# Performance work log

Hardware: AMD Instinct MI355X
Metric: run time of the kernel (lower is better)

Reference implementation:

```python
import jax, jax.numpy as jnp
from jax import lax
import numpy as np

WIN = 7            # skimage structural_similarity default win_size
K1, K2 = 0.01, 0.03
DATA_RANGE = 1.0


def _mean_filter_valid(x, win):
    k = jnp.ones((1, 1, win, win), x.dtype) / (win * win)
    y = lax.conv_general_dilated(x[:, None], k, (1, 1), 'VALID')
    return y[:, 0]


def ssim_loss(img1, img2):
    # img1, img2: (B, H, W); skimage-style SSIM, mean over batch of (1 - ssim)
    f = lambda z: _mean_filter_valid(z, WIN)
    NP = WIN * WIN
    cov_norm = NP / (NP - 1.0)  # unbiased estimator, as in skimage
    ux, uy = f(img1), f(img2)
    uxx, uyy, uxy = f(img1 * img1), f(img2 * img2), f(img1 * img2)
    vx = cov_norm * (uxx - ux * ux)
    vy = cov_norm * (uyy - uy * uy)
    vxy = cov_norm * (uxy - ux * uy)
    C1 = (K1 * DATA_RANGE) ** 2
    C2 = (K2 * DATA_RANGE) ** 2
    S = ((2 * ux * uy + C1) * (2 * vxy + C2)) / ((ux * ux + uy * uy + C1) * (vx + vy + C2))
    return jnp.mean(1.0 - jnp.mean(S, axis=(1, 2)))


def conv2d_same(x, w, b):
    # x: (B, Cin, H, W), w: (Cout, Cin, 3, 3)
    y = lax.conv_general_dilated(x, w, (1, 1), 'SAME')
    return y + b[None, :, None, None]


def maxpool2(x):
    return lax.reduce_window(x, -jnp.inf, lax.max, (1, 1, 2, 2), (1, 1, 2, 2), 'VALID')


def features(x, w1, b1, w2, b2, w3, b3, w4, b4):
    h = jax.nn.relu(conv2d_same(x, w1, b1))
    h = jax.nn.relu(conv2d_same(h, w2, b2))
    h = maxpool2(h)
    h = jax.nn.relu(conv2d_same(h, w3, b3))
    h = jax.nn.relu(conv2d_same(h, w4, b4))
    return h


def _conv_init(key, cout, cin, k=3):
    # torch Conv2d default init: U(-s, s), s = 1/sqrt(cin*k*k)
    kw, kb = jax.random.split(key)
    s = 1.0 / np.sqrt(cin * k * k)
    w = jax.random.uniform(kw, (cout, cin, k, k), jnp.float32, -s, s)
    b = jax.random.uniform(kb, (cout,), jnp.float32, -s, s)
    return w, b


def setup_inputs() -> dict:
    key = jax.random.key(0)
    ks = jax.random.split(key, 6)
    B, H, W = 8, 256, 256
    sr = jax.random.uniform(ks[0], (B, 1, H, W), jnp.float32)
    hr = jax.random.uniform(ks[1], (B, 1, H, W), jnp.float32)
    w1, b1 = _conv_init(ks[2], 64, 1)
    w2, b2 = _conv_init(ks[3], 128, 64)
    w3, b3 = _conv_init(ks[4], 256, 128)
    w4, b4 = _conv_init(ks[5], 256, 256)
    return {"sr": sr, "hr": hr, "w1": w1, "b1": b1, "w2": w2, "b2": b2,
            "w3": w3, "b3": b3, "w4": w4, "b4": b4}


def reference(sr, hr, w1, b1, w2, b2, w3, b3, w4, b4):
    mse_weight, ssim_weight, perceptual_weight = 1.0, 0.5, 0.1
    mse = jnp.mean((sr - hr) ** 2)
    # torch detaches before SSIM (numpy round-trip) -> no gradient through SSIM
    ssim_l = ssim_loss(lax.stop_gradient(sr[:, 0]), lax.stop_gradient(hr[:, 0]))
    sr_f = features(sr, w1, b1, w2, b2, w3, b3, w4, b4)
    hr_f = features(hr, w1, b1, w2, b2, w3, b3, w4, b4)
    perceptual = jnp.mean((sr_f - hr_f) ** 2)
    total = mse_weight * mse + ssim_weight * ssim_l + perceptual_weight * perceptual
    return total, mse, ssim_l, perceptual
```

## Files before the change

### kernel.cpp

```cpp
#include <hip/hip_runtime.h>
#include <hip/hip_bf16.h>

typedef __hip_bfloat16 bf16;
typedef unsigned char u8;
typedef __attribute__((ext_vector_type(4))) float f32x4;
typedef __attribute__((ext_vector_type(8))) int i32x8;
typedef __attribute__((ext_vector_type(4))) unsigned int u32x4;

struct L4 { long a, b, c, d; };
struct U2 { u32x4 x, y; };

typedef __attribute__((address_space(3))) unsigned int lds_uint;
typedef __attribute__((address_space(1))) const unsigned int g_uint;
__device__ inline void gload_lds16(const void* g, void* l) {
    __builtin_amdgcn_global_load_lds((g_uint*)g, (lds_uint*)l, 16, 0, 0);
}

__device__ inline void block_reduce_atomic(float v, float* dst) {
    #pragma unroll
    for (int o = 32; o > 0; o >>= 1) v += __shfl_down(v, o, 64);
    __shared__ float ws[8];
    const int lane = threadIdx.x & 63;
    const int wid  = threadIdx.x >> 6;
    if (lane == 0) ws[wid] = v;
    __syncthreads();
    if (threadIdx.x == 0) {
        float s = 0.f;
        const int nw = (blockDim.x + 63) >> 6;
        for (int i = 0; i < nw; ++i) s += ws[i];
        atomicAdd(dst, s);
    }
}

__global__ void prep_loss_kernel(
    const float* __restrict__ w2, u8* __restrict__ wb2,
    const float* __restrict__ w3, u8* __restrict__ wb3,
    const float* __restrict__ w4, u8* __restrict__ wb4,
    const float* __restrict__ x, const float* __restrict__ y,
    float* __restrict__ accs) {
    const int blk = blockIdx.x;
    if (blk < 3744) {
        const float* w; u8* wb; int CIN, CO, idx;
        if (blk < 288)       { w = w2; wb = wb2; CIN = 64;  CO = 128; idx = blk * 256 + threadIdx.x; }
        else if (blk < 1440) { w = w3; wb = wb3; CIN = 128; CO = 256; idx = (blk - 288) * 256 + threadIdx.x; }
        else                 { w = w4; wb = wb4; CIN = 256; CO = 256; idx = (blk - 1440) * 256 + threadIdx.x; }
        int n = CO * 9 * CIN;
        if (idx >= n) return;
        int t = idx % 9;
        int rest = idx / 9;
        int ci = rest % CIN;
        int co = rest / CIN;
        float v = w[idx];
        int p = ci >> 5, c32 = ci & 31;
        size_t off = (size_t)p * 288 * CO;
        if (t < 8) off += (((size_t)t * 2 + (c32 >> 4)) * CO + co) * 16 + (c32 & 15);
        else       off += 256 * (size_t)CO + (((size_t)(c32 >> 4)) * CO + co) * 16 + (c32 & 15);
        int r = __builtin_amdgcn_cvt_pk_fp8_f32(v, v, 0, false);
        wb[off] = (u8)(r & 0xff);
        return;
    }
    const int lb = blk - 3744;
    float val = 0.f;
    float* dst;
    if (lb < 1960) {
        dst = accs + 1;
        const int b = lb / 245;
        const int t = (lb - b * 245) * 256 + threadIdx.x;
        if (t < 250 * 250) {
            const int i = t / 250, j = t - (t / 250) * 250;
            const float* xp = x + (size_t)b * 65536;
            const float* yp = y + (size_t)b * 65536;
            float sx = 0.f, sy = 0.f, sxx = 0.f, syy = 0.f, sxy = 0.f;
            #pragma unroll
            for (int dy = 0; dy < 7; ++dy) {
                const float* xr = xp + (size_t)(i + dy) * 256 + j;
                const float* yr = yp + (size_t)(i + dy) * 256 + j;
                #pragma unroll
                for (int dx = 0; dx < 7; ++dx) {
                    float a = xr[dx], c = yr[dx];
                    sx += a; sy += c;
                    sxx += a * a; syy += c * c; sxy += a * c;
                }
            }
            const float inv = 1.f / 49.f;
            const float cn  = 49.f / 48.f;
            float ux = sx * inv, uy = sy * inv;
            float vx  = cn * (sxx * inv - ux * ux);
            float vy  = cn * (syy * inv - uy * uy);
            float vxy = cn * (sxy * inv - ux * uy);
            const float C1 = 1e-4f, C2 = 9e-4f;
            val = ((2.f * ux * uy + C1) * (2.f * vxy + C2)) /
                  ((ux * ux + uy * uy + C1) * (vx + vy + C2));
        }
    } else {
        dst = accs + 0;
        int i = (lb - 1960) * 256 + threadIdx.x;
        float4 a = ((const float4*)x)[i];
        float4 b = ((const float4*)y)[i];
        float d0 = a.x - b.x, d1 = a.y - b.y, d2 = a.z - b.z, d3 = a.w - b.w;
        val = d0 * d0 + d1 * d1 + d2 * d2 + d3 * d3;
    }
    block_reduce_atomic(val, dst);
}

__global__ void finalize_kernel(const float* __restrict__ accs, float* __restrict__ out) {
    if (threadIdx.x == 0) {
        float mse    = accs[0] * (1.f / 524288.f);
        float ssim_l = 1.f - accs[1] * (1.f / 500000.f);
        float perc   = accs[2] * (1.f / 33554432.f);
        out[0] = mse + 0.5f * ssim_l + 0.1f * perc;
        out[1] = mse;
        out[2] = ssim_l;
        out[3] = perc;
    }
}

__global__ __launch_bounds__(256) void conv1_kernel(
    const float* __restrict__ sr, const float* __restrict__ hr, int nb, int b0,
    const float* __restrict__ w, const float* __restrict__ bias,
    u8* __restrict__ out) {
    const int H = 256, W = 256;
    const int img = blockIdx.y;
    const float* in = (img < nb) ? (sr + (size_t)(b0 + img) * 65536)
                                 : (hr + (size_t)(b0 + img - nb) * 65536);
    int px = blockIdx.x * 256 + threadIdx.x;
    int y = px >> 8, x = px & 255;
    float p[9];
    #pragma unroll
    for (int dy = 0; dy < 3; ++dy)
        #pragma unroll
        for (int dx = 0; dx < 3; ++dx) {
            int gy = y + dy - 1, gx = x + dx - 1;
            float v = 0.f;
            if ((unsigned)gy < (unsigned)H && (unsigned)gx < (unsigned)W)
                v = in[(size_t)gy * W + gx];
            p[dy * 3 + dx] = v;
        }
    #pragma unroll
    for (int g = 0; g < 8; ++g) {
        float v[8];
        #pragma unroll
        for (int c = 0; c < 8; ++c) {
            int co = g * 8 + c;
            float a = bias[co];
            #pragma unroll
            for (int k = 0; k < 9; ++k) a += w[co * 9 + k] * p[k];
            v[c] = fmaxf(a, 0.f);
        }
        uint2 o;
        int r;
        r = __builtin_amdgcn_cvt_pk_fp8_f32(v[0], v[1], 0, false);
        o.x = __builtin_amdgcn_cvt_pk_fp8_f32(v[2], v[3], r, true);
        r = __builtin_amdgcn_cvt_pk_fp8_f32(v[4], v[5], 0, false);
        o.y = __builtin_amdgcn_cvt_pk_fp8_f32(v[6], v[7], r, true);
        *(uint2*)(out + (((size_t)img * 8 + g) * 65536 + px) * 8) = o;
    }
}

#define BUF_SZ   32768
#define N_ACT_CH 720
#define N_CHUNK  1872
#define WT_BOFF  11520

__global__ __launch_bounds__(256, 2) void conv2_ss(
    const u8* __restrict__ in, const u8* __restrict__ wb,
    const float* __restrict__ bias, u8* __restrict__ out,
    const float* __restrict__ zbuf) {
    const int H = 256, W = 256, CO = 128;
    const size_t HW = 65536;
    const int tid  = threadIdx.x;
    const int lane = tid & 63;
    const int wn   = tid >> 6;
    const int xl = lane & 15;
    const int kq = lane >> 4;
    const int x0 = blockIdx.x * 16;
    const int y0 = blockIdx.y * 16;
    const int img = blockIdx.z >> 1;
    const int co0 = (blockIdx.z & 1) << 6;

    __shared__ __align__(16) char smem[59904];

    f32x4 acc[4][4];
    #pragma unroll
    for (int m = 0; m < 4; ++m)
        #pragma unroll
        for (int n = 0; n < 4; ++n) acc[m][n] = (f32x4){0.f, 0.f, 0.f, 0.f};

    const u8* inp = in + (size_t)img * 8 * HW * 8;

    {
        char* d = smem + tid * 16;
        #pragma unroll
        for (int i = 0; i < 15; ++i) {
            int c = tid + i * 256;
            if (c >= 2 * N_CHUNK) break;
            int ph = (c >= N_CHUNK) ? 1 : 0;
            int c2 = c - ph * N_CHUNK;
            const char* src = (const char*)zbuf;
            if (c2 < N_ACT_CH) {
                int g = c2 / 180, r = c2 - g * 180;
                int row = r / 10, pp = r - row * 10;
                int gy = y0 - 1 + row, colb = x0 - 2 + pp * 2;
                if ((unsigned)gy < (unsigned)H && (unsigned)colb < (unsigned)(W - 1))
                    src = (const char*)(inp + (((size_t)(g + ph * 4)) * HW +
                                              (size_t)gy * W + colb) * 8);
            } else {
                int c3 = c2 - N_ACT_CH;
                size_t o;
                if (c3 < 1024) {
                    int gt = c3 >> 6, co = c3 & 63;
                    o = ((size_t)gt * CO + co0 + co) * 16;
                } else {
                    int c4 = c3 - 1024;
                    int q = c4 >> 6, co = c4 & 63;
                    o = 256 * (size_t)CO + ((size_t)q * CO + co0 + co) * 16;
                }
                src = (const char*)(wb + (size_t)ph * 288 * CO + o);
            }
            gload_lds16(src, d + i * 4096);
        }
    }

    int mxo[2];
    #pragma unroll
    for (int g = 0; g < 2; ++g) {
        int t = g * 4 + kq;
        int dy = t / 3, dx = t - dy * 3;
        mxo[g] = (dy * 20 + dx) * 8;
    }
    const int abase = ((wn * 4) * 20 + xl + 1) * 8;
    const int awmx  = WT_BOFF + kq * 2048 + xl * 16;
    const int aw8   = WT_BOFF + 16384 + (kq >> 1) * 1024 + xl * 16 + (kq & 1) * 8;
    const int ab8   = kq * 2880 + abase + (2 * 20 + 2) * 8;

    __syncthreads();

    #pragma unroll
    for (int p = 0; p < 2; ++p) {
        const char* base = smem + p * 29952;
        #pragma unroll
        for (int g = 0; g < 2; ++g) {
            i32x8 A[4];
            #pragma unroll
            for (int mt = 0; mt < 4; ++mt) {
                const char* pa = base + awmx + g * 8192 + mt * 256;
                U2 u{*(const u32x4*)pa, *(const u32x4*)(pa + 1024)};
                A[mt] = __builtin_bit_cast(i32x8, u);
            }
            #pragma unroll
            for (int nt = 0; nt < 4; ++nt) {
                const char* pb = base + abase + mxo[g] + nt * 160;
                L4 l{*(const long*)pb, *(const long*)(pb + 2880),
                     *(const long*)(pb + 5760), *(const long*)(pb + 8640)};
                i32x8 B = __builtin_bit_cast(i32x8, l);
                #pragma unroll
                for (int mt = 0; mt < 4; ++mt)
                    acc[mt][nt] = __builtin_amdgcn_mfma_scale_f32_16x16x128_f8f6f4(
                        A[mt], B, acc[mt][nt], 0, 0,
                        0, 0x7F7F7F7F, 0, 0x7F7F7F7F);
            }
        }
        {
            long A8[4], B8[4];
            #pragma unroll
            for (int mt = 0; mt < 4; ++mt)
                A8[mt] = *(const long*)(base + aw8 + mt * 256);
            #pragma unroll
            for (int nt = 0; nt < 4; ++nt)
                B8[nt] = *(const long*)(base + ab8 + nt * 160);
            #pragma unroll
            for (int mt = 0; mt < 4; ++mt)
                #pragma unroll
                for (int nt = 0; nt < 4; ++nt)
                    acc[mt][nt] = __builtin_amdgcn_mfma_f32_16x16x32_fp8_fp8(
                        A8[mt], B8[nt], acc[mt][nt], 0, 0, 0);
        }
    }

    const int Hp = H >> 1, Wp = W >> 1;
    const size_t HWp = (size_t)Hp * Wp;
    #pragma unroll
    for (int j = 0; j < 2; ++j) {
        const int py = (y0 + wn * 4 + 2 * j) >> 1;
        const int px = (x0 + xl) >> 1;
        #pragma unroll
        for (int mt = 0; mt < 4; ++mt) {
            const int cb = co0 + mt * 16 + kq * 4;
            const f32x4 bv = *(const f32x4*)(bias + cb);
            float v[4];
            #pragma unroll
            for (int r = 0; r < 4; ++r) {
                float a = acc[mt][2 * j][r] + bv[r];
                float b = acc[mt][2 * j + 1][r] + bv[r];
                float m = fmaxf(a, b);
                m = fmaxf(m, __shfl_xor(m, 1));
                v[r] = fmaxf(m, 0.f);
            }
            if (!(lane & 1)) {
                int w0 = __builtin_amdgcn_cvt_pk_fp8_f32(v[0], v[1], 0, false);
                w0 = __builtin_amdgcn_cvt_pk_fp8_f32(v[2], v[3], w0, true);
                *(int*)(out + (((size_t)img * (CO >> 4) + (cb >> 4)) * HWp +
                               (size_t)py * Wp + px) * 16 + (cb & 15)) = w0;
            }
        }
    }
}

#define C4_ACT  10368
#define C4_WT   20736
#define C4_BUF  39168
#define C4_NCH  2448

template <int NPH, int EPI, int IMGSH>
__global__ __launch_bounds__(256, 2) void conv34_fused(
    char* __restrict__ wsb,
    unsigned inOff,
    unsigned wOff,
    unsigned zOff,
    const float* __restrict__ bias,
    unsigned inHrOff,
    unsigned outOff,
    unsigned outHrOff,
    float* __restrict__ pacc) {
    const int tid  = threadIdx.x;
    const int lane = tid & 63;
    const int wn   = tid >> 6;
    const int xl = lane & 15;
    const int kq = lane >> 4;
    const int x0 = blockIdx.x * 16;
    const int y0 = blockIdx.y * 16;
    const int img = blockIdx.z >> 2;
    const int co0 = (blockIdx.z & 3) << 6;

    __shared__ __align__(16) char smem[2 * C4_BUF];

    f32x4 accS[4][4], accH[4][4];
    #pragma unroll
    for (int m = 0; m < 4; ++m)
        #pragma unroll
        for (int n = 0; n < 4; ++n) {
            accS[m][n] = (f32x4){0.f, 0.f, 0.f, 0.f};
            accH[m][n] = (f32x4){0.f, 0.f, 0.f, 0.f};
        }

    const unsigned inoff = inOff + ((unsigned)img << IMGSH);

    unsigned off[10];
    #pragma unroll
    for (int i = 0; i < 10; ++i) {
        int c = tid + i * 256;
        off[i] = zOff;
        if (c < 1296) {
            int c2 = (c >= 648) ? c - 648 : c;
            int g2 = c2 / 324, rem = c2 - g2 * 324;
            int row = rem / 18, col = rem - row * 18;
            int gy = y0 - 1 + row, gx = x0 - 1 + col;
            if ((unsigned)gy < 128u && (unsigned)gx < 128u)
                off[i] = inoff + ((c >= 648) ? inHrOff : 0u) +
                         (unsigned)((g2 * 16384 + gy * 128 + gx) * 16);
        } else if (c < C4_NCH) {
            int c3 = c - 1296;
            unsigned o;
            if (c3 < 1024) {
                int kblk = c3 >> 6, co = c3 & 63;
                o = (unsigned)((kblk * 256 + co0 + co) * 16);
            } else {
                int c4 = c3 - 1024;
                int h = c4 >> 6, co = c4 & 63;
                o = 65536u + (unsigned)((h * 256 + co0 + co) * 16);
            }
            off[i] = wOff + o;
        }
    }

    int bmx[2];
    #pragma unroll
    for (int g = 0; g < 2; ++g) {
        int t = g * 4 + kq;
        int dy = t / 3, dx = t - dy * 3;
        bmx[g] = (dy * 18 + dx) * 16;
    }
    const int bnt0 = ((wn * 4) * 18 + xl) * 16;
    const int awmx = C4_WT + kq * 2048 + xl * 16;
    const int aw8  = C4_WT + 16384 + (kq >> 1) * 1024 + xl * 16 + (kq & 1) * 8;
    const int ab8  = ((wn * 4 + 2) * 18 + xl + 2) * 16 +
                     (kq >> 1) * 5184 + (kq & 1) * 8;

#define C4_STAGE(DB) do {                                                   \
        char* d_ = (DB) + tid * 16;                                         \
        _Pragma("unroll")                                                   \
        for (int i_ = 0; i_ < 10; ++i_) {                                   \
            if (i_ < 9 || tid < 144) {                                      \
                gload_lds16(wsb + off[i_], d_ + i_ * 4096);                 \
                if (i_ < 5 || (i_ == 5 && tid < 16)) {                      \
                    if (off[i_] != zOff) off[i_] += 524288u;                \
                } else {                                                    \
                    off[i_] += 73728u;                                      \
                }                                                           \
            }                                                               \
        } } while (0)

    C4_STAGE(smem);

    for (int pp = 0; pp < NPH; ++pp) {
        __syncthreads();
        if (pp < NPH - 1) C4_STAGE(smem + ((pp + 1) & 1) * C4_BUF);
        const char* base = smem + (pp & 1) * C4_BUF;
        const char* aS = base;
        const char* aH = base + C4_ACT;
        __builtin_amdgcn_s_setprio(1);
        #pragma unroll
        for (int g = 0; g < 2; ++g) {
            i32x8 A[4];
            #pragma unroll
            for (int mt = 0; mt < 4; ++mt) {
                const char* pa = base + awmx + g * 8192 + mt * 256;
                U2 u{*(const u32x4*)pa, *(const u32x4*)(pa + 1024)};
                A[mt] = __builtin_bit_cast(i32x8, u);
            }
            #pragma unroll
            for (int nt = 0; nt < 4; ++nt) {
                const int bo = bnt0 + nt * 288 + bmx[g];
                U2 us{*(const u32x4*)(aS + bo), *(const u32x4*)(aS + bo + 5184)};
                i32x8 BS = __builtin_bit_cast(i32x8, us);
                #pragma unroll
                for (int mt = 0; mt < 4; ++mt)
                    accS[mt][nt] = __builtin_amdgcn_mfma_scale_f32_16x16x128_f8f6f4(
                        A[mt], BS, accS[mt][nt], 0, 0,
                        0, 0x7F7F7F7F, 0, 0x7F7F7F7F);
                U2 uh{*(const u32x4*)(aH + bo), *(const u32x4*)(aH + bo + 5184)};
                i32x8 BH = __builtin_bit_cast(i32x8, uh);
                #pragma unroll
                for (int mt = 0; mt < 4; ++mt)
                    accH[mt][nt] = __builtin_amdgcn_mfma_scale_f32_16x16x128_f8f6f4(
                        A[mt], BH, accH[mt][nt], 0, 0,
                        0, 0x7F7F7F7F, 0, 0x7F7F7F7F);
            }
        }
        {
            long A8[4];
            #pragma unroll
            for (int mt = 0; mt < 4; ++mt)
                A8[mt] = *(const long*)(base + aw8 + mt * 256);
            #pragma unroll
            for (int nt = 0; nt < 4; ++nt) {
                long bs = *(const long*)(aS + ab8 + nt * 288);
                long bh = *(const long*)(aH + ab8 + nt * 288);
                #pragma unroll
                for (int mt = 0; mt < 4; ++mt) {
                    accS[mt][nt] = __builtin_amdgcn_mfma_f32_16x16x32_fp8_fp8(
                        A8[mt], bs, accS[mt][nt], 0, 0, 0);
                    accH[mt][nt] = __builtin_amdgcn_mfma_f32_16x16x32_fp8_fp8(
                        A8[mt], bh, accH[mt][nt], 0, 0, 0);
                }
            }
        }
        __builtin_amdgcn_s_setprio(0);
    }
#undef C4_STAGE

    if (EPI == 0) {
        #pragma unroll
        for (int nt = 0; nt < 4; ++nt) {
            const int y = y0 + wn * 4 + nt;
            #pragma unroll
            for (int mt = 0; mt < 4; ++mt) {
                const int cb = co0 + mt * 16 + kq * 4;
                const f32x4 bv = *(const f32x4*)(bias + cb);
                const unsigned po = (unsigned)(((cb >> 4) * 16384 +
                                    y * 128 + x0 + xl) * 16 + (cb & 15));
                float v[4];
                #pragma unroll
                for (int r = 0; r < 4; ++r) v[r] = fmaxf(accS[mt][nt][r] + bv[r], 0.f);
                int w0 = __builtin_amdgcn_cvt_pk_fp8_f32(v[0], v[1], 0, false);
                w0 = __builtin_amdgcn_cvt_pk_fp8_f32(v[2], v[3], w0, true);
                *(int*)(wsb + outOff + ((unsigned)img << 22) + po) = w0;
                #pragma unroll
                for (int r = 0; r < 4; ++r) v[r] = fmaxf(accH[mt][nt][r] + bv[r], 0.f);
                w0 = __builtin_amdgcn_cvt_pk_fp8_f32(v[0], v[1], 0, false);
                w0 = __builtin_amdgcn_cvt_pk_fp8_f32(v[2], v[3], w0, true);
                *(int*)(wsb + outOff + outHrOff + ((unsigned)img << 22) + po) = w0;
            }
        }
    } else {
        float s = 0.f;
        #pragma unroll
        for (int mt = 0; mt < 4; ++mt) {
            const int cb = co0 + mt * 16 + kq * 4;
            const f32x4 bv = *(const f32x4*)(bias + cb);
            #pragma unroll
            for (int nt = 0; nt < 4; ++nt) {
                #pragma unroll
                for (int r = 0; r < 4; ++r) {
                    float vs = fmaxf(accS[mt][nt][r] + bv[r], 0.f);
                    float vh = fmaxf(accH[mt][nt][r] + bv[r], 0.f);
                    float d = vs - vh;
                    s += d * d;
                }
            }
        }
        #pragma unroll
        for (int o = 32; o > 0; o >>= 1) s += __shfl_down(s, o, 64);
        __syncthreads();
        if (lane == 0) *(float*)(smem + wn * 4) = s;
        __syncthreads();
        if (tid == 0) {
            float tot = *(float*)(smem) + *(float*)(smem + 4) +
                        *(float*)(smem + 8) + *(float*)(smem + 12);
            atomicAdd(pacc, tot);
        }
    }
}

extern "C" void kernel_launch(void* const* d_in, const int* in_sizes, int n_in,
                              void* d_out, int out_size, void* d_ws, size_t ws_size,
                              hipStream_t stream) {
    const float* sr = (const float*)d_in[0];
    const float* hr = (const float*)d_in[1];
    const float* w1 = (const float*)d_in[2];
    const float* b1 = (const float*)d_in[3];
    const float* w2 = (const float*)d_in[4];
    const float* b2 = (const float*)d_in[5];
    const float* w3 = (const float*)d_in[6];
    const float* b3 = (const float*)d_in[7];
    const float* w4 = (const float*)d_in[8];
    const float* b4 = (const float*)d_in[9];
    float* out = (float*)d_out;

    char* ws = (char*)d_ws;
    size_t off = 0;
    float* accs = (float*)(ws + off); off += 256;
    float* zbuf = (float*)(ws + off); off += 256;
    u8* wb2 = (u8*)(ws + off); off += (size_t)128 * 9 * 64;
    u8* wb3 = (u8*)(ws + off); off += (size_t)256 * 9 * 128;
    u8* wb4 = (u8*)(ws + off); off += (size_t)256 * 9 * 256;
    const size_t fixed = (off + 255) & ~(size_t)255;

    const size_t MB = 1024u * 1024u;
    int nb = 8;
    while (nb > 1 && fixed + (size_t)nb * 12 * MB > ws_size) nb >>= 1;

    u8* A = (u8*)(ws + fixed);
    u8* P = (u8*)(ws + fixed + (size_t)nb * 8 * MB);

    const unsigned zOffU = (unsigned)((char*)zbuf - ws);
    const unsigned aOffU = (unsigned)fixed;
    const unsigned pOffU = (unsigned)(fixed + (size_t)nb * 8 * MB);

    hipMemsetAsync(ws, 0, 512, stream);
    prep_loss_kernel<<<6216, 256, 0, stream>>>(w2, wb2, w3, wb3, w4, wb4, sr, hr, accs);

    for (int b0 = 0; b0 < 8; b0 += nb) {
        const int ni = 2 * nb;
        conv1_kernel<<<dim3(256, ni), 256, 0, stream>>>(sr, hr, nb, b0, w1, b1, A);
        conv2_ss<<<dim3(16, 16, ni * 2), 256, 0, stream>>>(A, wb2, b2, P, zbuf);
        conv34_fused<4, 0, 21><<<dim3(8, 8, nb * 4), 256, 0, stream>>>(
            ws, pOffU, (unsigned)((char*)wb3 - ws), zOffU, b3,
            (unsigned)nb << 21, aOffU, (unsigned)nb << 22, nullptr);
        conv34_fused<8, 1, 22><<<dim3(8, 8, nb * 4), 256, 0, stream>>>(
            ws, aOffU, (unsigned)((char*)wb4 - ws), zOffU, b4,
            (unsigned)nb << 22, 0u, 0u, accs + 2);
    }

    finalize_kernel<<<1, 1, 0, stream>>>(accs, out);
}
```

Measured before the change: 387.3 us.

## Fold conv1 into prep kernel and stagger conv34 block starts with sleeps

```diff
diff --git a/kernel.cpp b/kernel.cpp
--- a/kernel.cpp
+++ b/kernel.cpp
@@ -37,8 +37,49 @@
     const float* __restrict__ w3, u8* __restrict__ wb3,
     const float* __restrict__ w4, u8* __restrict__ wb4,
     const float* __restrict__ x, const float* __restrict__ y,
-    float* __restrict__ accs) {
+    float* __restrict__ accs,
+    const float* __restrict__ w1, const float* __restrict__ b1,
+    u8* __restrict__ aout) {
     const int blk = blockIdx.x;
+    if (blk >= 6216) {
+        const int lb2 = blk - 6216;
+        const int img = lb2 >> 8;
+        const float* in = (img < 8) ? (x + (size_t)img * 65536)
+                                    : (y + (size_t)(img - 8) * 65536);
+        const int px = ((lb2 & 255) << 8) + threadIdx.x;
+        const int yy = px >> 8, xx = px & 255;
+        float p[9];
+        #pragma unroll
+        for (int dy = 0; dy < 3; ++dy)
+            #pragma unroll
+            for (int dx = 0; dx < 3; ++dx) {
+                int gy = yy + dy - 1, gx = xx + dx - 1;
+                float v = 0.f;
+                if ((unsigned)gy < 256u && (unsigned)gx < 256u)
+                    v = in[(size_t)gy * 256 + gx];
+                p[dy * 3 + dx] = v;
+            }
+        #pragma unroll
+        for (int g = 0; g < 8; ++g) {
+            float v[8];
+            #pragma unroll
+            for (int c = 0; c < 8; ++c) {
+                int co = g * 8 + c;
+                float a = b1[co];
+                #pragma unroll
+                for (int k = 0; k < 9; ++k) a += w1[co * 9 + k] * p[k];
+                v[c] = fmaxf(a, 0.f);
+            }
+            uint2 o;
+            int r;
+            r = __builtin_amdgcn_cvt_pk_fp8_f32(v[0], v[1], 0, false);
+            o.x = __builtin_amdgcn_cvt_pk_fp8_f32(v[2], v[3], r, true);
+            r = __builtin_amdgcn_cvt_pk_fp8_f32(v[4], v[5], 0, false);
+            o.y = __builtin_amdgcn_cvt_pk_fp8_f32(v[6], v[7], r, true);
+            *(uint2*)(aout + (((size_t)img * 8 + g) * 65536 + px) * 8) = o;
+        }
+        return;
+    }
     if (blk < 3744) {
         const float* w; u8* wb; int CIN, CO, idx;
         if (blk < 288)       { w = w2; wb = wb2; CIN = 64;  CO = 128; idx = blk * 256 + threadIdx.x; }
@@ -332,6 +373,15 @@
     const int img = blockIdx.z >> 2;
     const int co0 = (blockIdx.z & 3) << 6;
 
+    {
+        unsigned h = ((unsigned)blockIdx.x * 0x9E3779B1u) ^
+                     ((unsigned)blockIdx.y * 0x85EBCA6Bu) ^
+                     ((unsigned)blockIdx.z * 0xC2B2AE35u);
+        int slp = (int)((h >> 20) & 63);
+        #pragma unroll 1
+        for (int i = 0; i < slp; ++i) __builtin_amdgcn_s_sleep(2);
+    }
+
     __shared__ __align__(16) char smem[2 * C4_BUF];
 
     f32x4 accS[4][4], accH[4][4];
@@ -547,12 +597,16 @@
     const unsigned aOffU = (unsigned)fixed;
     const unsigned pOffU = (unsigned)(fixed + (size_t)nb * 8 * MB);
 
+    const int c1n = (nb == 8) ? 4096 : 0;
+
     hipMemsetAsync(ws, 0, 512, stream);
-    prep_loss_kernel<<<6216, 256, 0, stream>>>(w2, wb2, w3, wb3, w4, wb4, sr, hr, accs);
+    prep_loss_kernel<<<6216 + c1n, 256, 0, stream>>>(
+        w2, wb2, w3, wb3, w4, wb4, sr, hr, accs, w1, b1, A);
 
     for (int b0 = 0; b0 < 8; b0 += nb) {
         const int ni = 2 * nb;
-        conv1_kernel<<<dim3(256, ni), 256, 0, stream>>>(sr, hr, nb, b0, w1, b1, A);
+        if (c1n == 0)
+            conv1_kernel<<<dim3(256, ni), 256, 0, stream>>>(sr, hr, nb, b0, w1, b1, A);
         conv2_ss<<<dim3(16, 16, ni * 2), 256, 0, stream>>>(A, wb2, b2, P, zbuf);
         conv34_fused<4, 0, 21><<<dim3(8, 8, nb * 4), 256, 0, stream>>>(
             ws, pOffU, (unsigned)((char*)wb3 - ws), zOffU, b3,
```

Result: no change. 392.3 us (+1.3%).
